# Kernel optimization log

Measured on AMD Instinct MI355X. Metric: run time of the kernel, lower is better.

## Reference

```python
import jax, jax.numpy as jnp
import numpy as np

B, K, D = 8192, 8192, 512

def setup_inputs() -> dict:
    key = jax.random.key(0)
    k1, k2 = jax.random.split(key)
    z_e = jax.random.normal(k1, (B, D), dtype=jnp.float32)
    # codebook: kaiming-uniform-initialized parameter; random normal scaled similarly is fine for a numeric baseline
    codebook = jax.random.normal(k2, (K, D), dtype=jnp.float32)
    return {"z_e": z_e, "codebook": codebook}

def reference(z_e, codebook):
    # Euclidean distances via dot-product expansion (same math as
    # torch.norm(z_e[:,None]-codebook[None], dim=-1) without the [B,K,D] intermediate):
    # d^2 = ||z||^2 - 2 z.c + ||c||^2
    z_sq = jnp.sum(z_e * z_e, axis=-1, keepdims=True)          # [B,1]
    c_sq = jnp.sum(codebook * codebook, axis=-1)               # [K]
    cross = jnp.einsum('bd,kd->bk', z_e, codebook)             # [B,K] GEMM
    d2 = jnp.maximum(z_sq - 2.0 * cross + c_sq[None, :], 0.0)  # clamp fp negatives
    distances = jnp.sqrt(d2)                                   # [B,K]
    indices = jnp.argmin(distances, axis=-1)                   # [B]
    z_q = jnp.take(codebook, indices, axis=0)                  # [B,D] gather
    return (z_q, indices)
```

## Files before the change

kernel.cpp:

```cpp
#include <hip/hip_runtime.h>


constexpr int Bn = 8192;
constexpr int Kn = 8192;
constexpr int Dn = 512;

using half8  = __attribute__((ext_vector_type(8)))  _Float16;
using f32x16 = __attribute__((ext_vector_type(16))) float;

#define WS_CSQ  0u
#define WS_ZSQ  (32u*1024u)
#define WS_MAX  (64u*1024u)
#define WS_CNT  (64u*1024u + 64u)
#define WS_WL   (96u*1024u)
#define WS_PART (1u*1024u*1024u)
#define WS_P2   WS_PART
#define WS_CIMG (10u*1024u*1024u)
#define WS_ZIMG (19u*1024u*1024u)

typedef __attribute__((address_space(3))) void       as3_void;
typedef const __attribute__((address_space(1))) void as1_cvoid;

#define MFMA16 __builtin_amdgcn_mfma_f32_32x32x16_f16


__global__ __launch_bounds__(256) void prep_kernel(const float* __restrict__ Z,
                                                   const float* __restrict__ Cb,
                                                   char* __restrict__ ws) {
  const int w = threadIdx.x >> 6, lane = threadIdx.x & 63;
  const int rid = blockIdx.x * 4 + w;
  if (blockIdx.x == 0 && threadIdx.x == 0) *(int*)(ws + WS_CNT) = 0;
  const bool isZ = rid < Bn;
  const int r = isZ ? rid : rid - Bn;
  const float* src = (isZ ? Z : Cb) + (size_t)r * Dn + lane * 8;
  const float4 v0 = *reinterpret_cast<const float4*>(src);
  const float4 v1 = *reinterpret_cast<const float4*>(src + 4);
  const float f[8] = {v0.x, v0.y, v0.z, v0.w, v1.x, v1.y, v1.z, v1.w};
  float ss = 0.f;
  _Float16 h[8];
#pragma unroll
  for (int j = 0; j < 8; ++j) { ss += f[j] * f[j]; h[j] = (_Float16)f[j]; }
#pragma unroll
  for (int off = 32; off; off >>= 1) ss += __shfl_xor(ss, off);
  const half8 vh = {h[0], h[1], h[2], h[3], h[4], h[5], h[6], h[7]};
  const int kt = lane >> 1, kh = lane & 1;
  int grp, rr, tbase, fr;
  char* img;
  if (isZ) {
    grp = (r >> 5) & 7; rr = r & 31; tbase = (r >> 8) * 33; fr = 512;
    img = ws + WS_ZIMG;
  } else {
    grp = (r >> 5) & 3; rr = r & 31; tbase = (r >> 7) * 33; fr = 256;
    img = ws + WS_CIMG;
  }
  const size_t chunk = (size_t)(tbase + kt) * fr + grp * 64 + kh * 32 + rr;
  *reinterpret_cast<half8*>(img + chunk * 16) = vh;
  if (lane < 2) {
    half8 ev = {0, 0, 0, 0, 0, 0, 0, 0};
    if (lane == 0) {
      if (isZ) { ev[0] = (_Float16)1.f; ev[1] = (_Float16)1.f; }
      else {
        const _Float16 hi = (_Float16)(-0.5f * ss);
        ev[0] = hi; ev[1] = (_Float16)(-0.5f * ss - (float)hi);
      }
    }
    const size_t ec = (size_t)(tbase + 32) * fr + grp * 64 + lane * 32 + rr;
    *reinterpret_cast<half8*>(img + ec * 16) = ev;
  }
  if (lane == 0) {
    if (isZ) ((float*)(ws + WS_ZSQ))[r] = ss;
    else {
      ((float*)(ws + WS_CSQ))[r] = ss;
      atomicMax((int*)(ws + WS_MAX), __float_as_int(ss));
    }
  }
}

__global__ __launch_bounds__(256, 2) void vq_pass1(char* __restrict__ ws) {
  __shared__ uint4 lds4[1536];
  char* lds = (char*)lds4;
  const int t = threadIdx.x, lane = t & 63, w = t >> 6;
  const int wm = w >> 1, wn = w & 1;
  const int zblk = blockIdx.x >> 4, split = blockIdx.x & 15;
  const int r31 = lane & 31, kh = lane >> 5;
  const char* CI = ws + WS_CIMG;
  const char* ZI = ws + WS_ZIMG;
  const size_t l16 = (size_t)lane * 16;
  const size_t zsrc = (size_t)zblk * 33 * 8192 + (size_t)w * 2048 + l16;
  const size_t abase = (size_t)(wm * 2) * 1024 + l16;

  float qs1[4], qs2[4];
  int qi1[4];
#pragma unroll
  for (int nb = 0; nb < 4; ++nb) { qs1[nb] = -3e38f; qs2[nb] = -3e38f; qi1[nb] = 0x7fffffff; }

  f32x16 acc[2][4] = {};
  half8 aA0, aA1, aB0, aB1;

  auto STAGE = [&](int kv, int bsel) {
    const char* s = ZI + zsrc + (size_t)kv * 8192;
    char* d = lds + bsel * 8192 + w * 2048;
    __builtin_amdgcn_global_load_lds((as1_cvoid*)(s), (as3_void*)(d), 16, 0, 0);
    __builtin_amdgcn_global_load_lds((as1_cvoid*)(s + 1024), (as3_void*)(d + 1024), 16, 0, 0);
  };

  STAGE(0, 0);
  STAGE(1, 1);
  {
    const char* s = CI + (size_t)(split * 4 * 33 + 0) * 4096 + abase;
    aA0 = *reinterpret_cast<const half8*>(s);
    aA1 = *reinterpret_cast<const half8*>(s + 1024);
  }
  asm volatile("s_waitcnt vmcnt(0)" ::: "memory");
  __builtin_amdgcn_s_barrier();

  int kt = 0, panel = 0, cur = 0, stg = 2;
#pragma unroll 2
  for (int u = 0; u < 132; ++u) {
    int k1 = kt + 1, p1 = panel;
    if (k1 == 33) { k1 = 0; ++p1; }
    int k2 = kt + 2, p2v = panel;
    if (k2 >= 33) { k2 -= 33; ++p2v; }
    if (u + 1 < 132) {
      const char* s = CI + (size_t)((split * 4 + p1) * 33 + k1) * 4096 + abase;
      if ((u & 1) == 0) {
        aB0 = *reinterpret_cast<const half8*>(s);
        aB1 = *reinterpret_cast<const half8*>(s + 1024);
      } else {
        aA0 = *reinterpret_cast<const half8*>(s);
        aA1 = *reinterpret_cast<const half8*>(s + 1024);
      }
    }
    if (u + 2 < 132) STAGE(k2, stg);
    const char* bb = lds + cur * 8192 + (size_t)wn * 4096 + l16;
    const half8 b0 = *reinterpret_cast<const half8*>(bb);
    const half8 b1 = *reinterpret_cast<const half8*>(bb + 1024);
    const half8 b2 = *reinterpret_cast<const half8*>(bb + 2048);
    const half8 b3 = *reinterpret_cast<const half8*>(bb + 3072);
    const half8 a0 = (u & 1) ? aB0 : aA0;
    const half8 a1 = (u & 1) ? aB1 : aA1;
    acc[0][0] = MFMA16(a0, b0, acc[0][0], 0, 0, 0);
    acc[0][1] = MFMA16(a0, b1, acc[0][1], 0, 0, 0);
    acc[0][2] = MFMA16(a0, b2, acc[0][2], 0, 0, 0);
    acc[0][3] = MFMA16(a0, b3, acc[0][3], 0, 0, 0);
    acc[1][0] = MFMA16(a1, b0, acc[1][0], 0, 0, 0);
    acc[1][1] = MFMA16(a1, b1, acc[1][1], 0, 0, 0);
    acc[1][2] = MFMA16(a1, b2, acc[1][2], 0, 0, 0);
    acc[1][3] = MFMA16(a1, b3, acc[1][3], 0, 0, 0);
    if (kt == 32) {
      const int cbase = split * 512 + panel * 128 + wm * 64 + 4 * kh;
#pragma unroll
      for (int nb = 0; nb < 4; ++nb) {
        float m1 = qs1[nb], m2 = qs2[nb];
        int i1 = qi1[nb];
#pragma unroll
        for (int ms = 0; ms < 2; ++ms)
#pragma unroll
          for (int r = 0; r < 16; ++r) {
            const float a = acc[ms][nb][r];
            const int ci = cbase + ms * 32 + (r & 3) + 8 * (r >> 2);
            const bool gt = (a > m1) || (a == m1 && ci < i1);
            const float nm2 = gt ? m1 : fmaxf(m2, a);
            m1 = gt ? a : m1;
            i1 = gt ? ci : i1;
            m2 = nm2;
          }
        qs1[nb] = m1; qs2[nb] = m2; qi1[nb] = i1;
      }
#pragma unroll
      for (int ms = 0; ms < 2; ++ms)
#pragma unroll
        for (int nb = 0; nb < 4; ++nb) acc[ms][nb] = (f32x16)0.f;
    }
    if (u < 130) asm volatile("s_waitcnt vmcnt(4)" ::: "memory");
    else         asm volatile("s_waitcnt vmcnt(2)" ::: "memory");
    __builtin_amdgcn_s_barrier();
    ++kt;
    if (kt == 33) { kt = 0; ++panel; }
    cur = (cur == 2) ? 0 : cur + 1;
    stg = (stg == 2) ? 0 : stg + 1;
  }

  float4* part = (float4*)(ws + WS_PART);
  const int bucket = split * 4 + wm * 2 + kh;
#pragma unroll
  for (int nb = 0; nb < 4; ++nb) {
    const int row = zblk * 256 + wn * 128 + nb * 32 + r31;
    part[(size_t)row * 64 + bucket] =
        make_float4(-2.f * qs1[nb], (float)qi1[nb], -2.f * qs2[nb], 0.f);
  }
}

__global__ __launch_bounds__(64) void gather_finalize(const float* __restrict__ Z,
                                                      const float* __restrict__ Cb,
                                                      char* __restrict__ ws,
                                                      float* __restrict__ zq,
                                                      float* __restrict__ idx_out) {
  const int row = blockIdx.x, l = threadIdx.x;
  const float4 q = ((const float4*)(ws + WS_PART))[(size_t)row * 64 + l];
  float s1 = q.x;
  int i1 = (int)q.y;
#pragma unroll
  for (int off = 1; off <= 32; off <<= 1) {
    const float os = __shfl_xor(s1, off); const int oi = __shfl_xor(i1, off);
    if (os < s1 || (os == s1 && oi < i1)) { s1 = os; i1 = oi; }
  }
  const float zs = ((const float*)(ws + WS_ZSQ))[row];
  const float cmax = __int_as_float(*(const int*)(ws + WS_MAX));
  const float thr = s1 + 4.0e-3f * sqrtf(zs * cmax) + 0.05f;
  int cnt = (q.x <= thr ? 1 : 0) + (q.z <= thr ? 1 : 0);
  int hide = (q.z <= thr) ? 1 : 0;
#pragma unroll
  for (int off = 1; off <= 32; off <<= 1) {
    cnt += __shfl_xor(cnt, off);
    hide |= __shfl_xor(hide, off);
  }
  if (cnt >= 5 || hide) {
    if (l == 0) {
      const int pos = atomicAdd((int*)(ws + WS_CNT), 1);
      if (pos < Bn) ((int*)(ws + WS_WL))[pos] = row;
    }
    return;
  }
  const float* csq = (const float*)(ws + WS_CSQ);
  const float4 z0 = *reinterpret_cast<const float4*>(Z + (size_t)row * Dn + l * 8);
  const float4 z1 = *reinterpret_cast<const float4*>(Z + (size_t)row * Dn + l * 8 + 4);
  float mycand = (q.x <= thr) ? q.x : 3e38f;
  const int myid = (int)q.y;
  float best_s = 3e38f;
  int best_i = 0x7fffffff;
  for (int it = 0; it < 4; ++it) {
    float cs_ = mycand;
    int ci_ = myid;
#pragma unroll
    for (int off = 1; off <= 32; off <<= 1) {
      const float os = __shfl_xor(cs_, off); const int oi = __shfl_xor(ci_, off);
      if (os < cs_ || (os == cs_ && oi < ci_)) { cs_ = os; ci_ = oi; }
    }
    if (cs_ > thr) break;
    if (myid == ci_) mycand = 3e38f;
    const float4 c0 = *reinterpret_cast<const float4*>(Cb + (size_t)ci_ * Dn + l * 8);
    const float4 c1 = *reinterpret_cast<const float4*>(Cb + (size_t)ci_ * Dn + l * 8 + 4);
    float pa = z0.x * c0.x + z0.y * c0.y + z0.z * c0.z + z0.w * c0.w +
               z1.x * c1.x + z1.y * c1.y + z1.z * c1.z + z1.w * c1.w;
#pragma unroll
    for (int off = 1; off <= 32; off <<= 1) pa += __shfl_xor(pa, off);
    const float se = csq[ci_] - 2.f * pa;
    if (se < best_s || (se == best_s && ci_ < best_i)) { best_s = se; best_i = ci_; }
  }
  const float4 o0 = *reinterpret_cast<const float4*>(Cb + (size_t)best_i * Dn + l * 8);
  const float4 o1 = *reinterpret_cast<const float4*>(Cb + (size_t)best_i * Dn + l * 8 + 4);
  *reinterpret_cast<float4*>(zq + (size_t)row * Dn + l * 8) = o0;
  *reinterpret_cast<float4*>(zq + (size_t)row * Dn + l * 8 + 4) = o1;
  if (l == 0) idx_out[row] = (float)best_i;
}

__global__ __launch_bounds__(256) void rescue1(const float* __restrict__ Z,
                                               const float* __restrict__ Cb,
                                               char* __restrict__ ws) {
  const int cntRaw = *(const int*)(ws + WS_CNT);
  const int cnt = cntRaw > Bn ? Bn : cntRaw;
  if (cnt == 0) return;
  const int tiles_r = (cnt + 63) >> 6;
  const int total = tiles_r * 128;
  const int* wl = (const int*)(ws + WS_WL);
  const float* csq = (const float*)(ws + WS_CSQ);
  float2* p2 = (float2*)(ws + WS_P2);
  __shared__ float As[32][68];
  __shared__ float Bs[32][68];
  __shared__ int wlrows[64];
  const int t = threadIdx.x;
  const int tx = t & 15, ty = t >> 4;
  const int sr = t >> 3, sc = (t & 7) * 4;
  for (int tile = blockIdx.x; tile < total; tile += gridDim.x) {
    const int tr = tile >> 7, tc = tile & 127;
    __syncthreads();
    if (t < 64) {
      const int wi = tr * 64 + t;
      wlrows[t] = wl[wi < cnt ? wi : cnt - 1];
    }
    __syncthreads();
    float acc[4][4] = {};
    for (int k0 = 0; k0 < Dn; k0 += 32) {
#pragma unroll
      for (int rr = 0; rr < 2; ++rr) {
        const int m = sr + rr * 32;
        const float4 v = *reinterpret_cast<const float4*>(Z + (size_t)wlrows[m] * Dn + k0 + sc);
        As[sc + 0][m] = v.x; As[sc + 1][m] = v.y; As[sc + 2][m] = v.z; As[sc + 3][m] = v.w;
        const float4 u = *reinterpret_cast<const float4*>(Cb + (size_t)(tc * 64 + m) * Dn + k0 + sc);
        Bs[sc + 0][m] = u.x; Bs[sc + 1][m] = u.y; Bs[sc + 2][m] = u.z; Bs[sc + 3][m] = u.w;
      }
      __syncthreads();
#pragma unroll
      for (int k = 0; k < 32; ++k) {
        const float4 a = *reinterpret_cast<const float4*>(&As[k][ty * 4]);
        const float4 b = *reinterpret_cast<const float4*>(&Bs[k][tx * 4]);
        acc[0][0] += a.x * b.x; acc[0][1] += a.x * b.y; acc[0][2] += a.x * b.z; acc[0][3] += a.x * b.w;
        acc[1][0] += a.y * b.x; acc[1][1] += a.y * b.y; acc[1][2] += a.y * b.z; acc[1][3] += a.y * b.w;
        acc[2][0] += a.z * b.x; acc[2][1] += a.z * b.y; acc[2][2] += a.z * b.z; acc[2][3] += a.z * b.w;
        acc[3][0] += a.w * b.x; acc[3][1] += a.w * b.y; acc[3][2] += a.w * b.z; acc[3][3] += a.w * b.w;
      }
      __syncthreads();
    }
#pragma unroll
    for (int i = 0; i < 4; ++i) {
      float bsv = 3e38f;
      int bi = 0;
#pragma unroll
      for (int j = 0; j < 4; ++j) {
        const int n = tc * 64 + tx * 4 + j;
        const float s = csq[n] - 2.f * acc[i][j];
        if (s < bsv || (s == bsv && n < bi)) { bsv = s; bi = n; }
      }
#pragma unroll
      for (int off = 1; off <= 8; off <<= 1) {
        const float os = __shfl_xor(bsv, off); const int oi = __shfl_xor(bi, off);
        if (os < bsv || (os == bsv && oi < bi)) { bsv = os; bi = oi; }
      }
      if (tx == 0) p2[(size_t)(tr * 64 + ty * 4 + i) * 128 + tc] = make_float2(bsv, (float)bi);
    }
  }
}

__global__ __launch_bounds__(64) void rescue2(const float* __restrict__ Cb,
                                              char* __restrict__ ws,
                                              float* __restrict__ zq,
                                              float* __restrict__ idx_out) {
  const int cntRaw = *(const int*)(ws + WS_CNT);
  const int cnt = cntRaw > Bn ? Bn : cntRaw;
  const int* wl = (const int*)(ws + WS_WL);
  const float2* p2 = (const float2*)(ws + WS_P2);
  const int l = threadIdx.x;
  for (int rr = blockIdx.x; rr < cnt; rr += gridDim.x) {
    const int row = wl[rr];
    const float2 e1 = p2[(size_t)rr * 128 + l];
    const float2 e2 = p2[(size_t)rr * 128 + 64 + l];
    float bs_ = e1.x;
    int bi_ = (int)e1.y;
    if (e2.x < bs_ || (e2.x == bs_ && (int)e2.y < bi_)) { bs_ = e2.x; bi_ = (int)e2.y; }
#pragma unroll
    for (int off = 1; off <= 32; off <<= 1) {
      const float os = __shfl_xor(bs_, off); const int oi = __shfl_xor(bi_, off);
      if (os < bs_ || (os == bs_ && oi < bi_)) { bs_ = os; bi_ = oi; }
    }
    const float4 c0 = *reinterpret_cast<const float4*>(Cb + (size_t)bi_ * Dn + l * 8);
    const float4 c1 = *reinterpret_cast<const float4*>(Cb + (size_t)bi_ * Dn + l * 8 + 4);
    *reinterpret_cast<float4*>(zq + (size_t)row * Dn + l * 8) = c0;
    *reinterpret_cast<float4*>(zq + (size_t)row * Dn + l * 8 + 4) = c1;
    if (l == 0) idx_out[row] = (float)bi_;
  }
}

extern "C" void kernel_launch(void* const* d_in, const int* in_sizes, int n_in,
                              void* d_out, int out_size, void* d_ws, size_t ws_size,
                              hipStream_t stream) {
  const float* Z = (const float*)d_in[0];
  const float* C = (const float*)d_in[1];
  float* out = (float*)d_out;
  char* ws = (char*)d_ws;

  prep_kernel<<<4096, 256, 0, stream>>>(Z, C, ws);
  vq_pass1<<<512, 256, 0, stream>>>(ws);
  gather_finalize<<<Bn, 64, 0, stream>>>(Z, C, ws, out, out + (size_t)Bn * Dn);
  rescue1<<<512, 256, 0, stream>>>(Z, C, ws);
  rescue2<<<256, 64, 0, stream>>>(C, ws, out, out + (size_t)Bn * Dn);
}
```

Baseline: 266.1 us.

## Split prep into sums and image kernels, deepen GEMM staging, remap blocks

Splits the prep kernel into a row-norm kernel and a separate fp16 image builder that writes coalesced 32-byte chunks per lane. The main MFMA loop now processes two k-steps per iteration with doubled LDS buffers and wraps compute in setprio. Blocks are remapped so consecutive blocks share codebook splits for L2 reuse. gather_finalize packs four rows per 256-thread block. Together these aim to cut prep write inefficiency, loop/barrier overhead and launch overhead, at the cost of an extra kernel launch and doubled LDS use (48KB/block).

```diff
diff --git a/kernel.cpp b/kernel.cpp
--- a/kernel.cpp
+++ b/kernel.cpp
@@ -24,9 +24,9 @@
 #define MFMA16 __builtin_amdgcn_mfma_f32_32x32x16_f16
 
 
-__global__ __launch_bounds__(256) void prep_kernel(const float* __restrict__ Z,
-                                                   const float* __restrict__ Cb,
-                                                   char* __restrict__ ws) {
+__global__ __launch_bounds__(256) void prep_sums(const float* __restrict__ Z,
+                                                 const float* __restrict__ Cb,
+                                                 char* __restrict__ ws) {
   const int w = threadIdx.x >> 6, lane = threadIdx.x & 63;
   const int rid = blockIdx.x * 4 + w;
   if (blockIdx.x == 0 && threadIdx.x == 0) *(int*)(ws + WS_CNT) = 0;
@@ -35,38 +35,10 @@
   const float* src = (isZ ? Z : Cb) + (size_t)r * Dn + lane * 8;
   const float4 v0 = *reinterpret_cast<const float4*>(src);
   const float4 v1 = *reinterpret_cast<const float4*>(src + 4);
-  const float f[8] = {v0.x, v0.y, v0.z, v0.w, v1.x, v1.y, v1.z, v1.w};
-  float ss = 0.f;
-  _Float16 h[8];
-#pragma unroll
-  for (int j = 0; j < 8; ++j) { ss += f[j] * f[j]; h[j] = (_Float16)f[j]; }
+  float ss = v0.x * v0.x + v0.y * v0.y + v0.z * v0.z + v0.w * v0.w +
+             v1.x * v1.x + v1.y * v1.y + v1.z * v1.z + v1.w * v1.w;
 #pragma unroll
   for (int off = 32; off; off >>= 1) ss += __shfl_xor(ss, off);
-  const half8 vh = {h[0], h[1], h[2], h[3], h[4], h[5], h[6], h[7]};
-  const int kt = lane >> 1, kh = lane & 1;
-  int grp, rr, tbase, fr;
-  char* img;
-  if (isZ) {
-    grp = (r >> 5) & 7; rr = r & 31; tbase = (r >> 8) * 33; fr = 512;
-    img = ws + WS_ZIMG;
-  } else {
-    grp = (r >> 5) & 3; rr = r & 31; tbase = (r >> 7) * 33; fr = 256;
-    img = ws + WS_CIMG;
-  }
-  const size_t chunk = (size_t)(tbase + kt) * fr + grp * 64 + kh * 32 + rr;
-  *reinterpret_cast<half8*>(img + chunk * 16) = vh;
-  if (lane < 2) {
-    half8 ev = {0, 0, 0, 0, 0, 0, 0, 0};
-    if (lane == 0) {
-      if (isZ) { ev[0] = (_Float16)1.f; ev[1] = (_Float16)1.f; }
-      else {
-        const _Float16 hi = (_Float16)(-0.5f * ss);
-        ev[0] = hi; ev[1] = (_Float16)(-0.5f * ss - (float)hi);
-      }
-    }
-    const size_t ec = (size_t)(tbase + 32) * fr + grp * 64 + lane * 32 + rr;
-    *reinterpret_cast<half8*>(img + ec * 16) = ev;
-  }
   if (lane == 0) {
     if (isZ) ((float*)(ws + WS_ZSQ))[r] = ss;
     else {
@@ -76,109 +48,173 @@
   }
 }
 
+__global__ __launch_bounds__(256) void prep_img(const float* __restrict__ Z,
+                                                const float* __restrict__ Cb,
+                                                char* __restrict__ ws) {
+  const int w = threadIdx.x >> 6, lane = threadIdx.x & 63;
+  const int wid = blockIdx.x * 4 + w;
+  char* CI = ws + WS_CIMG;
+  char* ZI = ws + WS_ZIMG;
+  if (wid < 2048) {
+    const bool isC = wid < 1024;
+    const int f = isC ? wid : wid - 1024;
+    const int koct = f & 3;
+    const int grp = isC ? ((f >> 2) & 3) : ((f >> 2) & 7);
+    const int blk = isC ? (f >> 4) : (f >> 5);
+    const int rowbase = (isC ? blk * 128 : blk * 256) + grp * 32;
+    const float* src = isC ? Cb : Z;
+    char* img = isC ? CI : ZI;
+    const int fr = isC ? 256 : 512;
+    const int ktsel = lane & 1, rr = lane >> 1;
+    const float* rowp = src + (size_t)(rowbase + rr) * Dn;
+#pragma unroll
+    for (int kp = 0; kp < 4; ++kp) {
+      const int kt = koct * 8 + kp * 2 + ktsel;
+      const float4 v0 = *reinterpret_cast<const float4*>(rowp + kt * 16);
+      const float4 v1 = *reinterpret_cast<const float4*>(rowp + kt * 16 + 4);
+      const float4 v2 = *reinterpret_cast<const float4*>(rowp + kt * 16 + 8);
+      const float4 v3 = *reinterpret_cast<const float4*>(rowp + kt * 16 + 12);
+      const float fl[16] = {v0.x, v0.y, v0.z, v0.w, v1.x, v1.y, v1.z, v1.w,
+                            v2.x, v2.y, v2.z, v2.w, v3.x, v3.y, v3.z, v3.w};
+      _Float16 h[16];
+#pragma unroll
+      for (int j = 0; j < 16; ++j) h[j] = (_Float16)fl[j];
+      const half8 lo8 = {h[0], h[1], h[2], h[3], h[4], h[5], h[6], h[7]};
+      const half8 hi8 = {h[8], h[9], h[10], h[11], h[12], h[13], h[14], h[15]};
+      char* fb = img + ((size_t)(blk * 33 + kt) * fr + grp * 64) * 16;
+      *reinterpret_cast<half8*>(fb + rr * 16) = lo8;
+      *reinterpret_cast<half8*>(fb + 512 + rr * 16) = hi8;
+    }
+  } else if (wid < 2304) {
+    const int e = wid - 2048;
+    const int grp = e & 3, blk = e >> 2;
+    half8 ev = {0, 0, 0, 0, 0, 0, 0, 0};
+    if (lane < 32) {
+      const float ss = ((const float*)(ws + WS_CSQ))[blk * 128 + grp * 32 + lane];
+      const _Float16 hi = (_Float16)(-0.5f * ss);
+      ev[0] = hi;
+      ev[1] = (_Float16)(-0.5f * ss - (float)hi);
+    }
+    char* fb = CI + ((size_t)(blk * 33 + 32) * 256 + grp * 64) * 16;
+    *reinterpret_cast<half8*>(fb + lane * 16) = ev;
+  } else if (wid < 2560) {
+    const int e = wid - 2304;
+    const int grp = e & 7, blk = e >> 3;
+    half8 ev = {0, 0, 0, 0, 0, 0, 0, 0};
+    if (lane < 32) { ev[0] = (_Float16)1.f; ev[1] = (_Float16)1.f; }
+    char* fb = ZI + ((size_t)(blk * 33 + 32) * 512 + grp * 64) * 16;
+    *reinterpret_cast<half8*>(fb + lane * 16) = ev;
+  }
+}
+
 __global__ __launch_bounds__(256, 2) void vq_pass1(char* __restrict__ ws) {
-  __shared__ uint4 lds4[1536];
+  __shared__ uint4 lds4[3072];
   char* lds = (char*)lds4;
   const int t = threadIdx.x, lane = t & 63, w = t >> 6;
   const int wm = w >> 1, wn = w & 1;
-  const int zblk = blockIdx.x >> 4, split = blockIdx.x & 15;
+  const int bid = blockIdx.x;
+  const int zblk = (bid & 7) * 4 + ((bid >> 3) & 3);
+  const int split = bid >> 5;
   const int r31 = lane & 31, kh = lane >> 5;
   const char* CI = ws + WS_CIMG;
   const char* ZI = ws + WS_ZIMG;
   const size_t l16 = (size_t)lane * 16;
-  const size_t zsrc = (size_t)zblk * 33 * 8192 + (size_t)w * 2048 + l16;
+  const size_t zbase = (size_t)zblk * 33 * 8192 + (size_t)w * 2048 + l16;
   const size_t abase = (size_t)(wm * 2) * 1024 + l16;
 
   float qs1[4], qs2[4];
   int qi1[4];
 #pragma unroll
   for (int nb = 0; nb < 4; ++nb) { qs1[nb] = -3e38f; qs2[nb] = -3e38f; qi1[nb] = 0x7fffffff; }
-
   f32x16 acc[2][4] = {};
-  half8 aA0, aA1, aB0, aB1;
-
-  auto STAGE = [&](int kv, int bsel) {
-    const char* s = ZI + zsrc + (size_t)kv * 8192;
-    char* d = lds + bsel * 8192 + w * 2048;
-    __builtin_amdgcn_global_load_lds((as1_cvoid*)(s), (as3_void*)(d), 16, 0, 0);
-    __builtin_amdgcn_global_load_lds((as1_cvoid*)(s + 1024), (as3_void*)(d + 1024), 16, 0, 0);
+
+  auto STAGE = [&](int u, int bsel) {
+#pragma unroll
+    for (int j = 0; j < 2; ++j) {
+      const int f = 2 * u + j;
+      const int k = f - (f / 33) * 33;
+      const char* s = ZI + zbase + (size_t)k * 8192;
+      char* d = lds + bsel * 16384 + j * 8192 + w * 2048;
+      __builtin_amdgcn_global_load_lds((as1_cvoid*)(s), (as3_void*)(d), 16, 0, 0);
+      __builtin_amdgcn_global_load_lds((as1_cvoid*)(s + 1024), (as3_void*)(d + 1024), 16, 0, 0);
+    }
   };
-
+  auto LOAD_A = [&](int u, half8 (&a)[4]) {
+#pragma unroll
+    for (int j = 0; j < 2; ++j) {
+      const int f = 2 * u + j;
+      const int p = f / 33, k = f - p * 33;
+      const char* s = CI + (size_t)((split * 4 + p) * 33 + k) * 4096 + abase;
+      a[j * 2 + 0] = *reinterpret_cast<const half8*>(s);
+      a[j * 2 + 1] = *reinterpret_cast<const half8*>(s + 1024);
+    }
+  };
+  auto FOLD = [&](int p) {
+    const int cbase = split * 512 + p * 128 + wm * 64 + 4 * kh;
+#pragma unroll
+    for (int nb = 0; nb < 4; ++nb) {
+      float m1 = qs1[nb], m2 = qs2[nb];
+      int i1 = qi1[nb];
+#pragma unroll
+      for (int ms = 0; ms < 2; ++ms)
+#pragma unroll
+        for (int r = 0; r < 16; ++r) {
+          const float a = acc[ms][nb][r];
+          const int ci = cbase + ms * 32 + (r & 3) + 8 * (r >> 2);
+          const bool gt = (a > m1) || (a == m1 && ci < i1);
+          const float nm2 = gt ? m1 : fmaxf(m2, a);
+          m1 = gt ? a : m1;
+          i1 = gt ? ci : i1;
+          m2 = nm2;
+        }
+      qs1[nb] = m1; qs2[nb] = m2; qi1[nb] = i1;
+    }
+#pragma unroll
+    for (int ms = 0; ms < 2; ++ms)
+#pragma unroll
+      for (int nb = 0; nb < 4; ++nb) acc[ms][nb] = (f32x16)0.f;
+  };
+
+  half8 aC[4], aN[4];
   STAGE(0, 0);
+  LOAD_A(0, aC);
   STAGE(1, 1);
-  {
-    const char* s = CI + (size_t)(split * 4 * 33 + 0) * 4096 + abase;
-    aA0 = *reinterpret_cast<const half8*>(s);
-    aA1 = *reinterpret_cast<const half8*>(s + 1024);
-  }
-  asm volatile("s_waitcnt vmcnt(0)" ::: "memory");
+  asm volatile("s_waitcnt vmcnt(4)" ::: "memory");
   __builtin_amdgcn_s_barrier();
 
-  int kt = 0, panel = 0, cur = 0, stg = 2;
-#pragma unroll 2
-  for (int u = 0; u < 132; ++u) {
-    int k1 = kt + 1, p1 = panel;
-    if (k1 == 33) { k1 = 0; ++p1; }
-    int k2 = kt + 2, p2v = panel;
-    if (k2 >= 33) { k2 -= 33; ++p2v; }
-    if (u + 1 < 132) {
-      const char* s = CI + (size_t)((split * 4 + p1) * 33 + k1) * 4096 + abase;
-      if ((u & 1) == 0) {
-        aB0 = *reinterpret_cast<const half8*>(s);
-        aB1 = *reinterpret_cast<const half8*>(s + 1024);
-      } else {
-        aA0 = *reinterpret_cast<const half8*>(s);
-        aA1 = *reinterpret_cast<const half8*>(s + 1024);
-      }
-    }
-    if (u + 2 < 132) STAGE(k2, stg);
-    const char* bb = lds + cur * 8192 + (size_t)wn * 4096 + l16;
-    const half8 b0 = *reinterpret_cast<const half8*>(bb);
-    const half8 b1 = *reinterpret_cast<const half8*>(bb + 1024);
-    const half8 b2 = *reinterpret_cast<const half8*>(bb + 2048);
-    const half8 b3 = *reinterpret_cast<const half8*>(bb + 3072);
-    const half8 a0 = (u & 1) ? aB0 : aA0;
-    const half8 a1 = (u & 1) ? aB1 : aA1;
-    acc[0][0] = MFMA16(a0, b0, acc[0][0], 0, 0, 0);
-    acc[0][1] = MFMA16(a0, b1, acc[0][1], 0, 0, 0);
-    acc[0][2] = MFMA16(a0, b2, acc[0][2], 0, 0, 0);
-    acc[0][3] = MFMA16(a0, b3, acc[0][3], 0, 0, 0);
-    acc[1][0] = MFMA16(a1, b0, acc[1][0], 0, 0, 0);
-    acc[1][1] = MFMA16(a1, b1, acc[1][1], 0, 0, 0);
-    acc[1][2] = MFMA16(a1, b2, acc[1][2], 0, 0, 0);
-    acc[1][3] = MFMA16(a1, b3, acc[1][3], 0, 0, 0);
-    if (kt == 32) {
-      const int cbase = split * 512 + panel * 128 + wm * 64 + 4 * kh;
-#pragma unroll
-      for (int nb = 0; nb < 4; ++nb) {
-        float m1 = qs1[nb], m2 = qs2[nb];
-        int i1 = qi1[nb];
-#pragma unroll
-        for (int ms = 0; ms < 2; ++ms)
-#pragma unroll
-          for (int r = 0; r < 16; ++r) {
-            const float a = acc[ms][nb][r];
-            const int ci = cbase + ms * 32 + (r & 3) + 8 * (r >> 2);
-            const bool gt = (a > m1) || (a == m1 && ci < i1);
-            const float nm2 = gt ? m1 : fmaxf(m2, a);
-            m1 = gt ? a : m1;
-            i1 = gt ? ci : i1;
-            m2 = nm2;
-          }
-        qs1[nb] = m1; qs2[nb] = m2; qi1[nb] = i1;
-      }
-#pragma unroll
-      for (int ms = 0; ms < 2; ++ms)
-#pragma unroll
-        for (int nb = 0; nb < 4; ++nb) acc[ms][nb] = (f32x16)0.f;
-    }
-    if (u < 130) asm volatile("s_waitcnt vmcnt(4)" ::: "memory");
-    else         asm volatile("s_waitcnt vmcnt(2)" ::: "memory");
+  auto BODY = [&](int u, half8 (&AU)[4], half8 (&AP)[4]) {
+    if (u + 1 < 66) LOAD_A(u + 1, AP);
+    if (u + 2 < 66) STAGE(u + 2, (u + 2) % 3);
+    const char* B0 = lds + (u % 3) * 16384 + (size_t)wn * 4096 + l16;
+    __builtin_amdgcn_s_setprio(1);
+#pragma unroll
+    for (int j = 0; j < 2; ++j) {
+      const char* bb = B0 + j * 8192;
+      const half8 b0 = *reinterpret_cast<const half8*>(bb);
+      const half8 b1 = *reinterpret_cast<const half8*>(bb + 1024);
+      const half8 b2 = *reinterpret_cast<const half8*>(bb + 2048);
+      const half8 b3 = *reinterpret_cast<const half8*>(bb + 3072);
+      acc[0][0] = MFMA16(AU[j * 2], b0, acc[0][0], 0, 0, 0);
+      acc[0][1] = MFMA16(AU[j * 2], b1, acc[0][1], 0, 0, 0);
+      acc[0][2] = MFMA16(AU[j * 2], b2, acc[0][2], 0, 0, 0);
+      acc[0][3] = MFMA16(AU[j * 2], b3, acc[0][3], 0, 0, 0);
+      acc[1][0] = MFMA16(AU[j * 2 + 1], b0, acc[1][0], 0, 0, 0);
+      acc[1][1] = MFMA16(AU[j * 2 + 1], b1, acc[1][1], 0, 0, 0);
+      acc[1][2] = MFMA16(AU[j * 2 + 1], b2, acc[1][2], 0, 0, 0);
+      acc[1][3] = MFMA16(AU[j * 2 + 1], b3, acc[1][3], 0, 0, 0);
+      const int f = 2 * u + j;
+      if (f - (f / 33) * 33 == 32) FOLD(f / 33);
+    }
+    __builtin_amdgcn_s_setprio(0);
+    if (u < 64)       asm volatile("s_waitcnt vmcnt(8)" ::: "memory");
+    else if (u == 64) asm volatile("s_waitcnt vmcnt(4)" ::: "memory");
+    else              asm volatile("s_waitcnt vmcnt(0)" ::: "memory");
     __builtin_amdgcn_s_barrier();
-    ++kt;
-    if (kt == 33) { kt = 0; ++panel; }
-    cur = (cur == 2) ? 0 : cur + 1;
-    stg = (stg == 2) ? 0 : stg + 1;
+  };
+
+  for (int up = 0; up < 33; ++up) {
+    BODY(2 * up, aC, aN);
+    BODY(2 * up + 1, aN, aC);
   }
 
   float4* part = (float4*)(ws + WS_PART);
@@ -191,12 +227,13 @@
   }
 }
 
-__global__ __launch_bounds__(64) void gather_finalize(const float* __restrict__ Z,
-                                                      const float* __restrict__ Cb,
-                                                      char* __restrict__ ws,
-                                                      float* __restrict__ zq,
-                                                      float* __restrict__ idx_out) {
-  const int row = blockIdx.x, l = threadIdx.x;
+__global__ __launch_bounds__(256) void gather_finalize(const float* __restrict__ Z,
+                                                       const float* __restrict__ Cb,
+                                                       char* __restrict__ ws,
+                                                       float* __restrict__ zq,
+                                                       float* __restrict__ idx_out) {
+  const int w = threadIdx.x >> 6, l = threadIdx.x & 63;
+  const int row = blockIdx.x * 4 + w;
   const float4 q = ((const float4*)(ws + WS_PART))[(size_t)row * 64 + l];
   float s1 = q.x;
   int i1 = (int)q.y;
@@ -359,9 +396,10 @@
   float* out = (float*)d_out;
   char* ws = (char*)d_ws;
 
-  prep_kernel<<<4096, 256, 0, stream>>>(Z, C, ws);
+  prep_sums<<<4096, 256, 0, stream>>>(Z, C, ws);
+  prep_img<<<640, 256, 0, stream>>>(Z, C, ws);
   vq_pass1<<<512, 256, 0, stream>>>(ws);
-  gather_finalize<<<Bn, 64, 0, stream>>>(Z, C, ws, out, out + (size_t)Bn * Dn);
+  gather_finalize<<<2048, 256, 0, stream>>>(Z, C, ws, out, out + (size_t)Bn * Dn);
   rescue1<<<512, 256, 0, stream>>>(Z, C, ws);
   rescue2<<<256, 64, 0, stream>>>(C, ws, out, out + (size_t)Bn * Dn);
 }
```

After: 619.2 us. 2.33x slower.
